# Performance work log

Hardware: AMD Instinct MI355X
Metric: run time of the kernel (lower is better)

## Reference

```python
import jax, jax.numpy as jnp
import numpy as np

N_SEQ, N_RES, C_M = 1024, 768, 64
NUM_HEAD = 8
HEAD_DIM = C_M // NUM_HEAD  # key_dim == value_dim == 8 per head
LARGE = 1e9
LN_EPS = 1e-5
MEAN_EPS = 1e-10


def setup_inputs() -> dict:
    key = jax.random.key(0)
    ks = jax.random.split(key, 8)
    msa_act = jax.random.normal(ks[0], (N_SEQ, N_RES, C_M), dtype=jnp.float32)
    msa_mask = (jax.random.uniform(ks[1], (N_SEQ, N_RES)) > 0.15).astype(jnp.float32)
    # fan-avg uniform init like VarianceScaling(1.0, 'fan_avg', 'uniform')
    def vs(k, shape, fan_in, fan_out):
        limit = jnp.sqrt(3.0 * 2.0 / (fan_in + fan_out))
        return jax.random.uniform(k, shape, minval=-limit, maxval=limit, dtype=jnp.float32)
    return {
        "msa_act": msa_act,
        "msa_mask": msa_mask,
        "ln_scale": jnp.ones((C_M,), jnp.float32),
        "ln_bias": jnp.zeros((C_M,), jnp.float32),
        "query_w": vs(ks[2], (C_M, NUM_HEAD, HEAD_DIM), C_M, NUM_HEAD * HEAD_DIM),
        "key_w": vs(ks[3], (C_M, HEAD_DIM), C_M, HEAD_DIM),
        "value_w": vs(ks[4], (C_M, HEAD_DIM), C_M, HEAD_DIM),
        "gating_w": jnp.zeros((C_M, NUM_HEAD, HEAD_DIM), jnp.float32),
        "gating_b": jnp.ones((NUM_HEAD, HEAD_DIM), jnp.float32),
        "output_w": vs(ks[5], (NUM_HEAD, HEAD_DIM, C_M), NUM_HEAD * HEAD_DIM, C_M),
        "output_b": jnp.zeros((C_M,), jnp.float32),
    }


def reference(msa_act, msa_mask, ln_scale, ln_bias, query_w, key_w, value_w,
              gating_w, gating_b, output_w, output_b):
    # permute: columns become the batch axis b = N_res
    x = jnp.transpose(msa_act, (1, 0, 2))          # [R, S, C]
    mask = jnp.transpose(msa_mask, (1, 0))[..., None]  # [R, S, 1]

    # LayerNorm over channels
    mu = jnp.mean(x, axis=-1, keepdims=True)
    var = jnp.mean(jnp.square(x - mu), axis=-1, keepdims=True)
    x = (x - mu) * jax.lax.rsqrt(var + LN_EPS) * ln_scale + ln_bias

    # shared (non-per-head) K/V projections
    v = jnp.einsum('bka,ac->bkc', x, value_w)      # [R, S, d]
    k = jnp.einsum('bka,ac->bkc', x, key_w)        # [R, S, d]

    # masked-mean single query per column
    q_avg = jnp.sum(mask * x, axis=1) / (jnp.sum(mask, axis=1) + MEAN_EPS)  # [R, C]
    q = jnp.einsum('ba,ahc->bhc', q_avg, query_w) * (HEAD_DIM ** -0.5)      # [R, H, d]

    bias = LARGE * (mask[:, None, :, 0] - 1.0)     # [R, 1, S]
    logits = jnp.einsum('bhc,bkc->bhk', q, k) + bias
    weights = jax.nn.softmax(logits, axis=-1)      # [R, H, S]
    weighted_avg = jnp.einsum('bhk,bkc->bhc', weights, v)  # [R, H, d]

    # sigmoid gating per (query, head, channel)
    gate = jax.nn.sigmoid(jnp.einsum('bqc,chv->bqhv', x, gating_w) + gating_b)  # [R, S, H, d]
    gated = weighted_avg[:, None] * gate           # [R, S, H, d]
    out = jnp.einsum('bqhc,hco->bqo', gated, output_w) + output_b  # [R, S, C]

    return jnp.transpose(out, (1, 0, 2))           # [S, R, C]
```

## Files before the change

kernel.cpp:

```cpp
#include <hip/hip_runtime.h>
#include <hip/hip_bf16.h>

#define N_S 1024
#define N_R 768
#define LN_EPS 1e-5f
#define MEAN_EPS 1e-10f
#define LARGE_F 1e9f
#define QSCALE 0.35355339059327373f

typedef __attribute__((ext_vector_type(8))) __bf16 bf16x8;
typedef __attribute__((ext_vector_type(4))) float f32x4;

__device__ __forceinline__ float bflo(unsigned u){ union{unsigned v; float f;} x; x.v = u << 16; return x.f; }
__device__ __forceinline__ unsigned short f2b(float f){
  __hip_bfloat16 h = __float2bfloat16(f);
  return *reinterpret_cast<unsigned short*>(&h);
}
__device__ __forceinline__ unsigned pk2(float a, float b){
  return (unsigned)f2b(a) | ((unsigned)f2b(b) << 16);
}
__device__ __forceinline__ bf16x8 ld_frag(const void* p){
  uint4 u = *reinterpret_cast<const uint4*>(p);
  return __builtin_bit_cast(bf16x8, u);
}

__device__ __forceinline__ void weight_prep(int wave, int lane,
    const float* __restrict__ gw, const float* __restrict__ ow, uint4* __restrict__ wsf)
{
  #pragma unroll 1
  for (int rep = 0; rep < 2; rep++) {
    int fi = wave + rep * 4;
    int mf = fi >> 1, ks = fi & 1;
    int g = lane >> 4, c15 = lane & 15;
    union { uint4 u; unsigned short h[8]; } ghi, glo, ohi, olo;
    #pragma unroll
    for (int t = 0; t < 8; t++) {
      int k = ks * 32 + g * 8 + t;
      float gv = gw[k * 64 + mf * 16 + c15];
      unsigned short gh = f2b(gv);
      ghi.h[t] = gh;
      glo.h[t] = f2b(gv - bflo(gh));
      float ov = ow[k * 64 + mf * 16 + c15];
      unsigned short oh = f2b(ov);
      ohi.h[t] = oh;
      olo.h[t] = f2b(ov - bflo(oh));
    }
    wsf[(0 * 8 + fi) * 64 + lane] = ghi.u;
    wsf[(1 * 8 + fi) * 64 + lane] = glo.u;
    wsf[(2 * 8 + fi) * 64 + lane] = ohi.u;
    wsf[(3 * 8 + fi) * 64 + lane] = olo.u;
  }
}

__global__ __launch_bounds__(256, 4) void lnkv_kernel(
    const float* __restrict__ act, const float* __restrict__ mask,
    const float* __restrict__ lns, const float* __restrict__ lnb,
    const float* __restrict__ kw,  const float* __restrict__ vw,
    const float* __restrict__ gw,  const float* __restrict__ ow,
    _Float16* __restrict__ kvws,   float* __restrict__ qpart,
    float* __restrict__ mpart,     uint4* __restrict__ wsf)
{
  __shared__ float redA[4][64];
  __shared__ float redB[4];

  const int tid  = threadIdx.x;
  const int lane = tid & 63;
  const int wave = tid >> 6;
  const int b    = blockIdx.x;

  if (b >= 3072) { weight_prep(wave, lane, gw, ow, wsf); return; }

  const int r  = b >> 2;
  const int sc = b & 3;
  const int s  = sc * 256 + tid;

  size_t base = ((size_t)s * N_R + r) * 64;
  float rw[64];
  const float4* rp = reinterpret_cast<const float4*>(act + base);
  #pragma unroll
  for (int i = 0; i < 16; i++) reinterpret_cast<float4*>(rw)[i] = rp[i];
  float m = mask[(size_t)s * N_R + r];

  float sum = 0.f, ss = 0.f;
  #pragma unroll
  for (int c = 0; c < 64; c++) { sum += rw[c]; ss += rw[c] * rw[c]; }
  float mu  = sum * (1.f / 64.f);
  float rsd = rsqrtf(ss * (1.f / 64.f) - mu * mu + LN_EPS);

  float kacc[8], vacc[8];
  #pragma unroll
  for (int d = 0; d < 8; d++) { kacc[d] = 0.f; vacc[d] = 0.f; }
  #pragma unroll
  for (int c = 0; c < 64; c++) {
    float xn = fmaf((rw[c] - mu) * rsd, lns[c], lnb[c]);
    rw[c] = xn;
    #pragma unroll
    for (int d = 0; d < 8; d++) {
      kacc[d] = fmaf(xn, kw[c * 8 + d], kacc[d]);
      vacc[d] = fmaf(xn, vw[c * 8 + d], vacc[d]);
    }
  }
  {
    union { uint4 u; _Float16 h[8]; } kb, vb;
    #pragma unroll
    for (int d = 0; d < 8; d++) { kb.h[d] = (_Float16)kacc[d]; vb.h[d] = (_Float16)vacc[d]; }
    _Float16* kvp = kvws + ((size_t)r * N_S + s) * 16;
    *reinterpret_cast<uint4*>(kvp)     = kb.u;
    *reinterpret_cast<uint4*>(kvp + 8) = vb.u;
  }

  float v[32];
  {
    const bool hi = (lane & 32) != 0;
    #pragma unroll
    for (int i = 0; i < 32; i++) {
      float gave = m * (hi ? rw[i] : rw[i + 32]);
      float keep = m * (hi ? rw[i + 32] : rw[i]);
      v[i] = keep + __shfl_xor(gave, 32);
    }
  }
  #pragma unroll
  for (int half = 16; half >= 1; half >>= 1) {
    const bool hi = (lane & half) != 0;
    #pragma unroll
    for (int i = 0; i < half; i++) {
      float gave = hi ? v[i] : v[i + half];
      float keep = hi ? v[i + half] : v[i];
      v[i] = keep + __shfl_xor(gave, half);
    }
  }
  float ms = m;
  #pragma unroll
  for (int o = 32; o > 0; o >>= 1) ms += __shfl_xor(ms, o);

  redA[wave][lane] = v[0];
  if (lane == 0) redB[wave] = ms;
  __syncthreads();
  if (tid < 64)
    qpart[((size_t)sc * N_R + r) * 64 + tid] =
        redA[0][tid] + redA[1][tid] + redA[2][tid] + redA[3][tid];
  if (tid == 64)
    mpart[sc * N_R + r] = redB[0] + redB[1] + redB[2] + redB[3];
}

__global__ __launch_bounds__(256, 2) void softmax_kernel(
    const float* __restrict__ mask, const float* __restrict__ qpart,
    const float* __restrict__ mpart, const float* __restrict__ qw,
    const _Float16* __restrict__ kvws, float* __restrict__ wavg_out)
{
  __shared__ float redA[4][64];
  __shared__ float redB[4][8];
  __shared__ float q_lds[64];
  __shared__ float qf_lds[64];

  const int tid  = threadIdx.x;
  const int lane = tid & 63;
  const int wave = tid >> 6;
  const int r    = blockIdx.x;

  if (tid < 64) {
    float qs = qpart[((size_t)0 * N_R + r) * 64 + tid] +
               qpart[((size_t)1 * N_R + r) * 64 + tid] +
               qpart[((size_t)2 * N_R + r) * 64 + tid] +
               qpart[((size_t)3 * N_R + r) * 64 + tid];
    float mt = mpart[0 * N_R + r] + mpart[1 * N_R + r] +
               mpart[2 * N_R + r] + mpart[3 * N_R + r];
    q_lds[tid] = qs / (mt + MEAN_EPS);
  }
  __syncthreads();
  if (tid < 64) {
    float acc = 0.f;
    for (int c = 0; c < 64; c++) acc = fmaf(q_lds[c], qw[c * 64 + tid], acc);
    qf_lds[tid] = acc * QSCALE;
  }
  __syncthreads();

  float qreg[64];
  #pragma unroll
  for (int j = 0; j < 64; j++) qreg[j] = qf_lds[j];

  float ev[4][8];
  float hm[8];
  #pragma unroll
  for (int h = 0; h < 8; h++) hm[h] = -1e30f;

  #pragma unroll
  for (int it = 0; it < 4; it++) {
    int s = tid + it * 256;
    union { uint4 u; _Float16 h[8]; } kb;
    kb.u = *reinterpret_cast<const uint4*>(kvws + ((size_t)r * N_S + s) * 16);
    float kk[8];
    #pragma unroll
    for (int d = 0; d < 8; d++) kk[d] = (float)kb.h[d];
    float m = mask[(size_t)s * N_R + r];
    float bias = LARGE_F * (m - 1.f);
    #pragma unroll
    for (int h = 0; h < 8; h++) {
      float l = bias;
      #pragma unroll
      for (int d = 0; d < 8; d++) l = fmaf(qreg[h * 8 + d], kk[d], l);
      ev[it][h] = l;
      hm[h] = fmaxf(hm[h], l);
    }
  }
  #pragma unroll
  for (int h = 0; h < 8; h++) {
    #pragma unroll
    for (int o = 32; o > 0; o >>= 1) hm[h] = fmaxf(hm[h], __shfl_xor(hm[h], o));
  }
  if (lane == 0) {
    #pragma unroll
    for (int h = 0; h < 8; h++) redB[wave][h] = hm[h];
  }
  __syncthreads();
  #pragma unroll
  for (int h = 0; h < 8; h++)
    hm[h] = fmaxf(fmaxf(redB[0][h], redB[1][h]), fmaxf(redB[2][h], redB[3][h]));
  __syncthreads();

  float hs[8];
  #pragma unroll
  for (int h = 0; h < 8; h++) hs[h] = 0.f;
  #pragma unroll
  for (int it = 0; it < 4; it++) {
    #pragma unroll
    for (int h = 0; h < 8; h++) {
      float e = __expf(ev[it][h] - hm[h]);
      ev[it][h] = e;
      hs[h] += e;
    }
  }
  #pragma unroll
  for (int h = 0; h < 8; h++) {
    #pragma unroll
    for (int o = 32; o > 0; o >>= 1) hs[h] += __shfl_xor(hs[h], o);
  }
  if (lane == 0) {
    #pragma unroll
    for (int h = 0; h < 8; h++) redB[wave][h] = hs[h];
  }
  __syncthreads();

  float wacc[64];
  #pragma unroll
  for (int j = 0; j < 64; j++) wacc[j] = 0.f;
  #pragma unroll
  for (int it = 0; it < 4; it++) {
    int s = tid + it * 256;
    union { uint4 u; _Float16 h[8]; } vb;
    vb.u = *reinterpret_cast<const uint4*>(kvws + ((size_t)r * N_S + s) * 16 + 8);
    float vv[8];
    #pragma unroll
    for (int d = 0; d < 8; d++) vv[d] = (float)vb.h[d];
    #pragma unroll
    for (int h = 0; h < 8; h++) {
      float w = ev[it][h];
      #pragma unroll
      for (int d = 0; d < 8; d++) wacc[h * 8 + d] = fmaf(w, vv[d], wacc[h * 8 + d]);
    }
  }
  #pragma unroll
  for (int j = 0; j < 64; j++) {
    #pragma unroll
    for (int o = 32; o > 0; o >>= 1) wacc[j] += __shfl_xor(wacc[j], o);
  }
  if (lane == 0) {
    #pragma unroll
    for (int j = 0; j < 64; j++) redA[wave][j] = wacc[j];
  }
  __syncthreads();
  if (tid < 64) {
    int h = tid >> 3;
    float hsv = redB[0][h] + redB[1][h] + redB[2][h] + redB[3][h];
    wavg_out[r * 64 + tid] =
        (redA[0][tid] + redA[1][tid] + redA[2][tid] + redA[3][tid]) / hsv;
  }
}

struct SharedS { _Float16 kv[N_S][16]; };

__global__ __launch_bounds__(256, 2) void stats_kernel(
    const float* __restrict__ act, const float* __restrict__ mask,
    const float* __restrict__ lns, const float* __restrict__ lnb,
    const float* __restrict__ qw,  const float* __restrict__ kw,
    const float* __restrict__ vw,  const float* __restrict__ gw,
    const float* __restrict__ ow,  float* __restrict__ wavg_out,
    uint4* __restrict__ wsf)
{
  __shared__ SharedS sh;
  __shared__ float redA[4][64];
  __shared__ float redB[4][8];
  __shared__ float q_lds[64];
  __shared__ float qf_lds[64];

  const int tid  = threadIdx.x;
  const int lane = tid & 63;
  const int wave = tid >> 6;
  const int r    = blockIdx.x;

  if (r >= N_R) { weight_prep(wave, lane, gw, ow, wsf); return; }

  float qacc[64];
  #pragma unroll
  for (int c = 0; c < 64; c++) qacc[c] = 0.f;
  float msum = 0.f;

  #pragma unroll 1
  for (int it = 0; it < 4; it++) {
    int s = tid + it * 256;
    size_t base = ((size_t)s * N_R + r) * 64;
    float rw[64];
    const float4* rp = reinterpret_cast<const float4*>(act + base);
    #pragma unroll
    for (int i = 0; i < 16; i++) reinterpret_cast<float4*>(rw)[i] = rp[i];
    float m = mask[(size_t)s * N_R + r];
    float sum = 0.f, ss = 0.f;
    #pragma unroll
    for (int c = 0; c < 64; c++) { sum += rw[c]; ss += rw[c] * rw[c]; }
    float mu  = sum * (1.f / 64.f);
    float rsd = rsqrtf(ss * (1.f / 64.f) - mu * mu + LN_EPS);
    float kacc[8], vacc[8];
    #pragma unroll
    for (int d = 0; d < 8; d++) { kacc[d] = 0.f; vacc[d] = 0.f; }
    #pragma unroll
    for (int c = 0; c < 64; c++) {
      float xn = fmaf((rw[c] - mu) * rsd, lns[c], lnb[c]);
      qacc[c] = fmaf(m, xn, qacc[c]);
      #pragma unroll
      for (int d = 0; d < 8; d++) {
        kacc[d] = fmaf(xn, kw[c * 8 + d], kacc[d]);
        vacc[d] = fmaf(xn, vw[c * 8 + d], vacc[d]);
      }
    }
    union { uint4 u; _Float16 h[8]; } kb, vb;
    #pragma unroll
    for (int d = 0; d < 8; d++) { kb.h[d] = (_Float16)kacc[d]; vb.h[d] = (_Float16)vacc[d]; }
    *reinterpret_cast<uint4*>(&sh.kv[s][0]) = kb.u;
    *reinterpret_cast<uint4*>(&sh.kv[s][8]) = vb.u;
    msum += m;
  }

  #pragma unroll
  for (int c = 0; c < 64; c++) {
    #pragma unroll
    for (int o = 32; o > 0; o >>= 1) qacc[c] += __shfl_xor(qacc[c], o);
  }
  #pragma unroll
  for (int o = 32; o > 0; o >>= 1) msum += __shfl_xor(msum, o);
  if (lane == 0) {
    redB[wave][0] = msum;
    #pragma unroll
    for (int c = 0; c < 64; c++) redA[wave][c] = qacc[c];
  }
  __syncthreads();
  if (tid < 64) {
    float qs = redA[0][tid] + redA[1][tid] + redA[2][tid] + redA[3][tid];
    float mt = redB[0][0] + redB[1][0] + redB[2][0] + redB[3][0];
    q_lds[tid] = qs / (mt + MEAN_EPS);
  }
  __syncthreads();
  if (tid < 64) {
    float acc = 0.f;
    for (int c = 0; c < 64; c++) acc = fmaf(q_lds[c], qw[c * 64 + tid], acc);
    qf_lds[tid] = acc * QSCALE;
  }
  __syncthreads();

  float qreg[64];
  #pragma unroll
  for (int j = 0; j < 64; j++) qreg[j] = qf_lds[j];
  float ev[4][8];
  float hm[8];
  #pragma unroll
  for (int h = 0; h < 8; h++) hm[h] = -1e30f;
  #pragma unroll
  for (int it = 0; it < 4; it++) {
    int s = tid + it * 256;
    union { uint4 u; _Float16 h[8]; } kb;
    kb.u = *reinterpret_cast<uint4*>(&sh.kv[s][0]);
    float kk[8];
    #pragma unroll
    for (int d = 0; d < 8; d++) kk[d] = (float)kb.h[d];
    float m = mask[(size_t)s * N_R + r];
    float bias = LARGE_F * (m - 1.f);
    #pragma unroll
    for (int h = 0; h < 8; h++) {
      float l = bias;
      #pragma unroll
      for (int d = 0; d < 8; d++) l = fmaf(qreg[h * 8 + d], kk[d], l);
      ev[it][h] = l;
      hm[h] = fmaxf(hm[h], l);
    }
  }
  #pragma unroll
  for (int h = 0; h < 8; h++) {
    #pragma unroll
    for (int o = 32; o > 0; o >>= 1) hm[h] = fmaxf(hm[h], __shfl_xor(hm[h], o));
  }
  if (lane == 0) {
    #pragma unroll
    for (int h = 0; h < 8; h++) redB[wave][h] = hm[h];
  }
  __syncthreads();
  #pragma unroll
  for (int h = 0; h < 8; h++)
    hm[h] = fmaxf(fmaxf(redB[0][h], redB[1][h]), fmaxf(redB[2][h], redB[3][h]));
  __syncthreads();

  float hs[8];
  #pragma unroll
  for (int h = 0; h < 8; h++) hs[h] = 0.f;
  #pragma unroll
  for (int it = 0; it < 4; it++) {
    #pragma unroll
    for (int h = 0; h < 8; h++) {
      float e = __expf(ev[it][h] - hm[h]);
      ev[it][h] = e;
      hs[h] += e;
    }
  }
  #pragma unroll
  for (int h = 0; h < 8; h++) {
    #pragma unroll
    for (int o = 32; o > 0; o >>= 1) hs[h] += __shfl_xor(hs[h], o);
  }
  if (lane == 0) {
    #pragma unroll
    for (int h = 0; h < 8; h++) redB[wave][h] = hs[h];
  }
  __syncthreads();

  float wacc[64];
  #pragma unroll
  for (int j = 0; j < 64; j++) wacc[j] = 0.f;
  #pragma unroll
  for (int it = 0; it < 4; it++) {
    int s = tid + it * 256;
    union { uint4 u; _Float16 h[8]; } vb;
    vb.u = *reinterpret_cast<uint4*>(&sh.kv[s][8]);
    float vv[8];
    #pragma unroll
    for (int d = 0; d < 8; d++) vv[d] = (float)vb.h[d];
    #pragma unroll
    for (int h = 0; h < 8; h++) {
      float w = ev[it][h];
      #pragma unroll
      for (int d = 0; d < 8; d++) wacc[h * 8 + d] = fmaf(w, vv[d], wacc[h * 8 + d]);
    }
  }
  #pragma unroll
  for (int j = 0; j < 64; j++) {
    #pragma unroll
    for (int o = 32; o > 0; o >>= 1) wacc[j] += __shfl_xor(wacc[j], o);
  }
  if (lane == 0) {
    #pragma unroll
    for (int j = 0; j < 64; j++) redA[wave][j] = wacc[j];
  }
  __syncthreads();
  if (tid < 64) {
    int h = tid >> 3;
    float hsv = redB[0][h] + redB[1][h] + redB[2][h] + redB[3][h];
    wavg_out[r * 64 + tid] =
        (redA[0][tid] + redA[1][tid] + redA[2][tid] + redA[3][tid]) / hsv;
  }
}

__device__ __forceinline__ void proj_tile(
    const float4 (&rv)[4], int t, int wv, int lane, int qr, int qc, int g, int c15,
    const float4 (&s4)[4], const float4 (&b4)[4],
    const float* __restrict__ gb, const float* __restrict__ ob,
    const float* __restrict__ wavg, const uint4 (*wfrag)[64],
    char* my, float* __restrict__ out)
{
  const int r  = t >> 4;
  const int s0 = ((t & 15) << 6) + wv * 16;

  float sum = 0.f, ssq = 0.f;
  #pragma unroll
  for (int i = 0; i < 4; i++) {
    sum += rv[i].x + rv[i].y + rv[i].z + rv[i].w;
    ssq += rv[i].x * rv[i].x + rv[i].y * rv[i].y + rv[i].z * rv[i].z + rv[i].w * rv[i].w;
  }
  sum += __shfl_xor(sum, 1); ssq += __shfl_xor(ssq, 1);
  sum += __shfl_xor(sum, 2); ssq += __shfl_xor(ssq, 2);
  float mu  = sum * (1.f / 64.f);
  float rsd = rsqrtf(ssq * (1.f / 64.f) - mu * mu + LN_EPS);

  #pragma unroll
  for (int i = 0; i < 4; i++) {
    float x0 = fmaf((rv[i].x - mu) * rsd, s4[i].x, b4[i].x);
    float x1 = fmaf((rv[i].y - mu) * rsd, s4[i].y, b4[i].y);
    float x2 = fmaf((rv[i].z - mu) * rsd, s4[i].z, b4[i].z);
    float x3 = fmaf((rv[i].w - mu) * rsd, s4[i].w, b4[i].w);
    uint2 p; p.x = pk2(x0, x1); p.y = pk2(x2, x3);
    int byt = ((2 * i + (qc >> 1)) << 8) + (qr << 4) + ((qc & 1) << 3);
    *reinterpret_cast<uint2*>(my + byt) = p;
  }
  asm volatile("" ::: "memory");
  bf16x8 xb0 = ld_frag(my + lane * 16);
  bf16x8 xb1 = ld_frag(my + 1024 + lane * 16);

  const f32x4 zero = {0.f, 0.f, 0.f, 0.f};
  f32x4 acc[4] = {zero, zero, zero, zero};
  #pragma unroll
  for (int mf = 0; mf < 4; mf++) {
    acc[mf] = __builtin_amdgcn_mfma_f32_16x16x32_bf16(ld_frag(&wfrag[     mf*2    ][lane]), xb0, acc[mf], 0, 0, 0);
    acc[mf] = __builtin_amdgcn_mfma_f32_16x16x32_bf16(ld_frag(&wfrag[ 8 + mf*2    ][lane]), xb0, acc[mf], 0, 0, 0);
    acc[mf] = __builtin_amdgcn_mfma_f32_16x16x32_bf16(ld_frag(&wfrag[     mf*2 + 1][lane]), xb1, acc[mf], 0, 0, 0);
    acc[mf] = __builtin_amdgcn_mfma_f32_16x16x32_bf16(ld_frag(&wfrag[ 8 + mf*2 + 1][lane]), xb1, acc[mf], 0, 0, 0);
  }

  asm volatile("" ::: "memory");
  #pragma unroll
  for (int mf = 0; mf < 4; mf++) {
    int jb = mf * 16 + 4 * g;
    float4 wv4 = *reinterpret_cast<const float4*>(wavg + r * 64 + jb);
    float4 gb4 = *reinterpret_cast<const float4*>(gb + jb);
    float c0 = wv4.x / (1.f + __expf(-(acc[mf][0] + gb4.x)));
    float c1 = wv4.y / (1.f + __expf(-(acc[mf][1] + gb4.y)));
    float c2 = wv4.z / (1.f + __expf(-(acc[mf][2] + gb4.z)));
    float c3 = wv4.w / (1.f + __expf(-(acc[mf][3] + gb4.w)));
    uint2 p; p.x = pk2(c0, c1); p.y = pk2(c2, c3);
    int byt = ((2 * mf + (g >> 1)) << 8) + (c15 << 4) + ((g & 1) << 3);
    *reinterpret_cast<uint2*>(my + byt) = p;
  }
  asm volatile("" ::: "memory");
  bf16x8 cb0 = ld_frag(my + lane * 16);
  bf16x8 cb1 = ld_frag(my + 1024 + lane * 16);

  f32x4 acc2[4] = {zero, zero, zero, zero};
  #pragma unroll
  for (int mf = 0; mf < 4; mf++) {
    acc2[mf] = __builtin_amdgcn_mfma_f32_16x16x32_bf16(ld_frag(&wfrag[16 + mf*2    ][lane]), cb0, acc2[mf], 0, 0, 0);
    acc2[mf] = __builtin_amdgcn_mfma_f32_16x16x32_bf16(ld_frag(&wfrag[24 + mf*2    ][lane]), cb0, acc2[mf], 0, 0, 0);
    acc2[mf] = __builtin_amdgcn_mfma_f32_16x16x32_bf16(ld_frag(&wfrag[16 + mf*2 + 1][lane]), cb1, acc2[mf], 0, 0, 0);
    acc2[mf] = __builtin_amdgcn_mfma_f32_16x16x32_bf16(ld_frag(&wfrag[24 + mf*2 + 1][lane]), cb1, acc2[mf], 0, 0, 0);
  }

  size_t obase = ((size_t)(s0 + c15) * N_R + r) * 64;
  #pragma unroll
  for (int mf = 0; mf < 4; mf++) {
    int o0 = mf * 16 + 4 * g;
    float4 e = *reinterpret_cast<const float4*>(ob + o0);
    float4 o4;
    o4.x = acc2[mf][0] + e.x;
    o4.y = acc2[mf][1] + e.y;
    o4.z = acc2[mf][2] + e.z;
    o4.w = acc2[mf][3] + e.w;
    *reinterpret_cast<float4*>(out + obase + o0) = o4;
  }
}

__global__ __launch_bounds__(256, 4) void proj_kernel(
    const float* __restrict__ act, const float* __restrict__ lns,
    const float* __restrict__ lnb, const float* __restrict__ gb,
    const float* __restrict__ ob,  const float* __restrict__ wavg,
    const uint4* __restrict__ wsf, float* __restrict__ out)
{
  __shared__ uint4 wfrag[32][64];
  __shared__ __align__(16) char wbuf[4][2048];

  const int tid  = threadIdx.x;
  const int lane = tid & 63;
  const int wv   = tid >> 6;
  const int b    = blockIdx.x;
  const int qr = lane >> 2, qc = lane & 3;
  const int g = lane >> 4, c15 = lane & 15;
  char* my = wbuf[wv];

  float4 rvA[4], rvB[4];
  {
    int t = b;
    const float4* ap = reinterpret_cast<const float4*>(
        act + ((size_t)((((t & 15) << 6) + wv * 16) + qr) * N_R + (t >> 4)) * 64);
    rvA[0] = ap[qc]; rvA[1] = ap[qc + 4]; rvA[2] = ap[qc + 8]; rvA[3] = ap[qc + 12];
  }

  {
    uint4* dst = &wfrag[0][0];
    #pragma unroll
    for (int i = 0; i < 8; i++) dst[tid + i * 256] = wsf[tid + i * 256];
  }

  float4 s4[4], b4[4];
  #pragma unroll
  for (int i = 0; i < 4; i++) {
    int c0 = 16 * i + 4 * qc;
    s4[i] = *reinterpret_cast<const float4*>(lns + c0);
    b4[i] = *reinterpret_cast<const float4*>(lnb + c0);
  }
  __syncthreads();

  #pragma unroll 1
  for (int i = 0; i < 12; i += 2) {
    {
      int t = (i + 1) * 1024 + b;
      const float4* ap = reinterpret_cast<const float4*>(
          act + ((size_t)((((t & 15) << 6) + wv * 16) + qr) * N_R + (t >> 4)) * 64);
      rvB[0] = ap[qc]; rvB[1] = ap[qc + 4]; rvB[2] = ap[qc + 8]; rvB[3] = ap[qc + 12];
    }
    proj_tile(rvA, i * 1024 + b, wv, lane, qr, qc, g, c15, s4, b4, gb, ob, wavg, wfrag, my, out);
    if (i + 2 < 12) {
      int t = (i + 2) * 1024 + b;
      const float4* ap = reinterpret_cast<const float4*>(
          act + ((size_t)((((t & 15) << 6) + wv * 16) + qr) * N_R + (t >> 4)) * 64);
      rvA[0] = ap[qc]; rvA[1] = ap[qc + 4]; rvA[2] = ap[qc + 8]; rvA[3] = ap[qc + 12];
    }
    proj_tile(rvB, (i + 1) * 1024 + b, wv, lane, qr, qc, g, c15, s4, b4, gb, ob, wavg, wfrag, my, out);
  }
}

extern "C" void kernel_launch(void* const* d_in, const int* in_sizes, int n_in,
                              void* d_out, int out_size, void* d_ws, size_t ws_size,
                              hipStream_t stream)
{
  const float* act  = (const float*)d_in[0];
  const float* mask = (const float*)d_in[1];
  const float* lns  = (const float*)d_in[2];
  const float* lnb  = (const float*)d_in[3];
  const float* qw   = (const float*)d_in[4];
  const float* kw   = (const float*)d_in[5];
  const float* vw   = (const float*)d_in[6];
  const float* gw   = (const float*)d_in[7];
  const float* gb   = (const float*)d_in[8];
  const float* ob   = (const float*)d_in[10];
  const float* ow   = (const float*)d_in[9];

  char* ws = (char*)d_ws;
  float* wavg_ws = (float*)ws;
  uint4* wsf     = (uint4*)(ws + 196608);
  const size_t OFF_KV = 229376;
  const size_t OFF_QP = OFF_KV + 25165824;
  const size_t OFF_MP = OFF_QP + 786432;
  const size_t NEED   = OFF_MP + 12288;

  if (ws_size >= NEED) {
    _Float16* kvws = (_Float16*)(ws + OFF_KV);
    float* qpart   = (float*)(ws + OFF_QP);
    float* mpart   = (float*)(ws + OFF_MP);
    lnkv_kernel<<<3073, 256, 0, stream>>>(act, mask, lns, lnb, kw, vw, gw, ow,
                                          kvws, qpart, mpart, wsf);
    softmax_kernel<<<N_R, 256, 0, stream>>>(mask, qpart, mpart, qw, kvws, wavg_ws);
  } else {
    stats_kernel<<<N_R + 1, 256, 0, stream>>>(act, mask, lns, lnb, qw, kw, vw,
                                              gw, ow, wavg_ws, wsf);
  }
  proj_kernel<<<1024, 256, 0, stream>>>(act, lns, lnb, gb, ob,
                                        wavg_ws, (const uint4*)wsf, (float*)d_out);
}
```

Baseline: 649.9 us.

## Split each LayerNorm row across two lanes in lnkv kernel

The lnkv kernel now assigns each (seq,res) row to a pair of lanes, each holding 32 channels, combining LN statistics and K/V partial sums with lane shuffles. This halves per-thread register use, doubles the grid, and shortens the butterfly reduction for the masked-mean query. Partial sums grow from 4 to 8 chunks, so softmax reads more partials. Separately, proj_kernel reloads LN scale and bias per tile instead of keeping them in registers, to relieve register pressure.

```diff
diff --git a/kernel.cpp b/kernel.cpp
--- a/kernel.cpp
+++ b/kernel.cpp
@@ -52,7 +52,7 @@
   }
 }
 
-__global__ __launch_bounds__(256, 4) void lnkv_kernel(
+__global__ __launch_bounds__(256, 2) void lnkv_kernel(
     const float* __restrict__ act, const float* __restrict__ mask,
     const float* __restrict__ lns, const float* __restrict__ lnb,
     const float* __restrict__ kw,  const float* __restrict__ vw,
@@ -68,22 +68,27 @@
   const int wave = tid >> 6;
   const int b    = blockIdx.x;
 
-  if (b >= 3072) { weight_prep(wave, lane, gw, ow, wsf); return; }
-
-  const int r  = b >> 2;
-  const int sc = b & 3;
-  const int s  = sc * 256 + tid;
-
-  size_t base = ((size_t)s * N_R + r) * 64;
-  float rw[64];
-  const float4* rp = reinterpret_cast<const float4*>(act + base);
-  #pragma unroll
-  for (int i = 0; i < 16; i++) reinterpret_cast<float4*>(rw)[i] = rp[i];
+  if (b >= 6144) { weight_prep(wave, lane, gw, ow, wsf); return; }
+
+  const int r  = b >> 3;
+  const int sc = b & 7;
+  const int s  = sc * 128 + (tid >> 1);
+  const int h  = tid & 1;
+
+  float rw[32];
+  {
+    const float4* rp = reinterpret_cast<const float4*>(
+        act + ((size_t)s * N_R + r) * 64 + h * 32);
+    #pragma unroll
+    for (int i = 0; i < 8; i++) reinterpret_cast<float4*>(rw)[i] = rp[i];
+  }
   float m = mask[(size_t)s * N_R + r];
 
   float sum = 0.f, ss = 0.f;
   #pragma unroll
-  for (int c = 0; c < 64; c++) { sum += rw[c]; ss += rw[c] * rw[c]; }
+  for (int i = 0; i < 32; i++) { sum += rw[i]; ss += rw[i] * rw[i]; }
+  sum += __shfl_xor(sum, 1);
+  ss  += __shfl_xor(ss, 1);
   float mu  = sum * (1.f / 64.f);
   float rsd = rsqrtf(ss * (1.f / 64.f) - mu * mu + LN_EPS);
 
@@ -91,49 +96,48 @@
   #pragma unroll
   for (int d = 0; d < 8; d++) { kacc[d] = 0.f; vacc[d] = 0.f; }
   #pragma unroll
-  for (int c = 0; c < 64; c++) {
-    float xn = fmaf((rw[c] - mu) * rsd, lns[c], lnb[c]);
-    rw[c] = xn;
+  for (int i = 0; i < 32; i++) {
+    int c = h * 32 + i;
+    float xn = fmaf((rw[i] - mu) * rsd, lns[c], lnb[c]);
+    rw[i] = m * xn;
     #pragma unroll
     for (int d = 0; d < 8; d++) {
       kacc[d] = fmaf(xn, kw[c * 8 + d], kacc[d]);
       vacc[d] = fmaf(xn, vw[c * 8 + d], vacc[d]);
     }
   }
+  #pragma unroll
+  for (int d = 0; d < 8; d++) {
+    kacc[d] += __shfl_xor(kacc[d], 1);
+    vacc[d] += __shfl_xor(vacc[d], 1);
+  }
   {
-    union { uint4 u; _Float16 h[8]; } kb, vb;
-    #pragma unroll
-    for (int d = 0; d < 8; d++) { kb.h[d] = (_Float16)kacc[d]; vb.h[d] = (_Float16)vacc[d]; }
-    _Float16* kvp = kvws + ((size_t)r * N_S + s) * 16;
-    *reinterpret_cast<uint4*>(kvp)     = kb.u;
-    *reinterpret_cast<uint4*>(kvp + 8) = vb.u;
-  }
-
-  float v[32];
+    union { uint4 u; _Float16 hh[8]; } pk;
+    #pragma unroll
+    for (int d = 0; d < 8; d++) pk.hh[d] = (_Float16)(h ? vacc[d] : kacc[d]);
+    *reinterpret_cast<uint4*>(kvws + ((size_t)r * N_S + s) * 16 + h * 8) = pk.u;
+  }
+
+  #pragma unroll
+  for (int half = 16; half >= 1; half >>= 1) {
+    const int stride = 32 / half;
+    const bool hi = (lane & stride) != 0;
+    #pragma unroll
+    for (int i = 0; i < half; i++) {
+      float gave = hi ? rw[i] : rw[i + half];
+      float keep = hi ? rw[i + half] : rw[i];
+      rw[i] = keep + __shfl_xor(gave, stride);
+    }
+  }
   {
-    const bool hi = (lane & 32) != 0;
-    #pragma unroll
-    for (int i = 0; i < 32; i++) {
-      float gave = m * (hi ? rw[i] : rw[i + 32]);
-      float keep = m * (hi ? rw[i + 32] : rw[i]);
-      v[i] = keep + __shfl_xor(gave, 32);
-    }
-  }
-  #pragma unroll
-  for (int half = 16; half >= 1; half >>= 1) {
-    const bool hi = (lane & half) != 0;
-    #pragma unroll
-    for (int i = 0; i < half; i++) {
-      float gave = hi ? v[i] : v[i + half];
-      float keep = hi ? v[i + half] : v[i];
-      v[i] = keep + __shfl_xor(gave, half);
-    }
-  }
-  float ms = m;
+    int local = (((lane >> 1) & 1) << 4) | (((lane >> 2) & 1) << 3) |
+                (((lane >> 3) & 1) << 2) | (((lane >> 4) & 1) << 1) |
+                ((lane >> 5) & 1);
+    redA[wave][h * 32 + local] = rw[0];
+  }
+  float ms = h ? 0.f : m;
   #pragma unroll
   for (int o = 32; o > 0; o >>= 1) ms += __shfl_xor(ms, o);
-
-  redA[wave][lane] = v[0];
   if (lane == 0) redB[wave] = ms;
   __syncthreads();
   if (tid < 64)
@@ -159,12 +163,12 @@
   const int r    = blockIdx.x;
 
   if (tid < 64) {
-    float qs = qpart[((size_t)0 * N_R + r) * 64 + tid] +
-               qpart[((size_t)1 * N_R + r) * 64 + tid] +
-               qpart[((size_t)2 * N_R + r) * 64 + tid] +
-               qpart[((size_t)3 * N_R + r) * 64 + tid];
-    float mt = mpart[0 * N_R + r] + mpart[1 * N_R + r] +
-               mpart[2 * N_R + r] + mpart[3 * N_R + r];
+    float qs = 0.f;
+    #pragma unroll
+    for (int p = 0; p < 8; p++) qs += qpart[((size_t)p * N_R + r) * 64 + tid];
+    float mt = 0.f;
+    #pragma unroll
+    for (int p = 0; p < 8; p++) mt += mpart[p * N_R + r];
     q_lds[tid] = qs / (mt + MEAN_EPS);
   }
   __syncthreads();
@@ -468,7 +472,7 @@
 
 __device__ __forceinline__ void proj_tile(
     const float4 (&rv)[4], int t, int wv, int lane, int qr, int qc, int g, int c15,
-    const float4 (&s4)[4], const float4 (&b4)[4],
+    const float* __restrict__ lns, const float* __restrict__ lnb,
     const float* __restrict__ gb, const float* __restrict__ ob,
     const float* __restrict__ wavg, const uint4 (*wfrag)[64],
     char* my, float* __restrict__ out)
@@ -489,10 +493,13 @@
 
   #pragma unroll
   for (int i = 0; i < 4; i++) {
-    float x0 = fmaf((rv[i].x - mu) * rsd, s4[i].x, b4[i].x);
-    float x1 = fmaf((rv[i].y - mu) * rsd, s4[i].y, b4[i].y);
-    float x2 = fmaf((rv[i].z - mu) * rsd, s4[i].z, b4[i].z);
-    float x3 = fmaf((rv[i].w - mu) * rsd, s4[i].w, b4[i].w);
+    int c0 = 16 * i + 4 * qc;
+    float4 s4 = *reinterpret_cast<const float4*>(lns + c0);
+    float4 b4 = *reinterpret_cast<const float4*>(lnb + c0);
+    float x0 = fmaf((rv[i].x - mu) * rsd, s4.x, b4.x);
+    float x1 = fmaf((rv[i].y - mu) * rsd, s4.y, b4.y);
+    float x2 = fmaf((rv[i].z - mu) * rsd, s4.z, b4.z);
+    float x3 = fmaf((rv[i].w - mu) * rsd, s4.w, b4.w);
     uint2 p; p.x = pk2(x0, x1); p.y = pk2(x2, x3);
     int byt = ((2 * i + (qc >> 1)) << 8) + (qr << 4) + ((qc & 1) << 3);
     *reinterpret_cast<uint2*>(my + byt) = p;
@@ -576,19 +583,10 @@
         act + ((size_t)((((t & 15) << 6) + wv * 16) + qr) * N_R + (t >> 4)) * 64);
     rvA[0] = ap[qc]; rvA[1] = ap[qc + 4]; rvA[2] = ap[qc + 8]; rvA[3] = ap[qc + 12];
   }
-
   {
     uint4* dst = &wfrag[0][0];
     #pragma unroll
     for (int i = 0; i < 8; i++) dst[tid + i * 256] = wsf[tid + i * 256];
-  }
-
-  float4 s4[4], b4[4];
-  #pragma unroll
-  for (int i = 0; i < 4; i++) {
-    int c0 = 16 * i + 4 * qc;
-    s4[i] = *reinterpret_cast<const float4*>(lns + c0);
-    b4[i] = *reinterpret_cast<const float4*>(lnb + c0);
   }
   __syncthreads();
 
@@ -600,14 +598,14 @@
           act + ((size_t)((((t & 15) << 6) + wv * 16) + qr) * N_R + (t >> 4)) * 64);
       rvB[0] = ap[qc]; rvB[1] = ap[qc + 4]; rvB[2] = ap[qc + 8]; rvB[3] = ap[qc + 12];
     }
-    proj_tile(rvA, i * 1024 + b, wv, lane, qr, qc, g, c15, s4, b4, gb, ob, wavg, wfrag, my, out);
+    proj_tile(rvA, i * 1024 + b, wv, lane, qr, qc, g, c15, lns, lnb, gb, ob, wavg, wfrag, my, out);
     if (i + 2 < 12) {
       int t = (i + 2) * 1024 + b;
       const float4* ap = reinterpret_cast<const float4*>(
           act + ((size_t)((((t & 15) << 6) + wv * 16) + qr) * N_R + (t >> 4)) * 64);
       rvA[0] = ap[qc]; rvA[1] = ap[qc + 4]; rvA[2] = ap[qc + 8]; rvA[3] = ap[qc + 12];
     }
-    proj_tile(rvB, (i + 1) * 1024 + b, wv, lane, qr, qc, g, c15, s4, b4, gb, ob, wavg, wfrag, my, out);
+    proj_tile(rvB, (i + 1) * 1024 + b, wv, lane, qr, qc, g, c15, lns, lnb, gb, ob, wavg, wfrag, my, out);
   }
 }
 
@@ -624,22 +622,22 @@
   const float* vw   = (const float*)d_in[6];
   const float* gw   = (const float*)d_in[7];
   const float* gb   = (const float*)d_in[8];
+  const float* ow   = (const float*)d_in[9];
   const float* ob   = (const float*)d_in[10];
-  const float* ow   = (const float*)d_in[9];
 
   char* ws = (char*)d_ws;
   float* wavg_ws = (float*)ws;
   uint4* wsf     = (uint4*)(ws + 196608);
   const size_t OFF_KV = 229376;
   const size_t OFF_QP = OFF_KV + 25165824;
-  const size_t OFF_MP = OFF_QP + 786432;
-  const size_t NEED   = OFF_MP + 12288;
+  const size_t OFF_MP = OFF_QP + 1572864;
+  const size_t NEED   = OFF_MP + 24576;
 
   if (ws_size >= NEED) {
     _Float16* kvws = (_Float16*)(ws + OFF_KV);
     float* qpart   = (float*)(ws + OFF_QP);
     float* mpart   = (float*)(ws + OFF_MP);
-    lnkv_kernel<<<3073, 256, 0, stream>>>(act, mask, lns, lnb, kw, vw, gw, ow,
+    lnkv_kernel<<<6145, 256, 0, stream>>>(act, mask, lns, lnb, kw, vw, gw, ow,
                                           kvws, qpart, mpart, wsf);
     softmax_kernel<<<N_R, 256, 0, stream>>>(mask, qpart, mpart, qw, kvws, wavg_ws);
   } else {
```

After: 662.3 us. Within noise of the previous version (+1.9%).
